# Optimization experiments

Measured on AMD Instinct MI355X. Metric: run time of the kernel, lower is better.

## Reference

```python
import jax, jax.numpy as jnp
import numpy as np

TAU_FILTER_INV = 1000.0
DT = 0.001
# decay = 1 - alpha = exp(-dt * tau_filter_inv)
DECAY = float(np.exp(-DT * TAU_FILTER_INV))


def setup_inputs() -> dict:
    key = jax.random.key(0)
    k1, k2, k3 = jax.random.split(key, 3)
    T, B, I, O = 2048, 32, 256, 256
    input_tensor = jax.random.normal(k1, (T, B, I), dtype=jnp.float32)
    # Linear weight init mimics uniform(-k, k), k = sqrt(1/input_size)
    k = float(np.sqrt(1.0 / I))
    W = jax.random.uniform(k2, (O, I), dtype=jnp.float32, minval=-k, maxval=k)
    b = jax.random.uniform(k3, (O,), dtype=jnp.float32, minval=-k, maxval=k)
    return {"input_tensor": input_tensor, "W": W, "b": b}


def reference(input_tensor, W, b):
    # Dense projection: [T, B, I] @ [I, O] -> [T, B, O]
    y = jnp.einsum("tbi,oi->tbo", input_tensor, W) + b
    decay = jnp.asarray(DECAY, dtype=y.dtype)

    # s(t) = y(t) + decay * s(t-1); s(0) = y(0) (init state 0)
    def step(s, x):
        s = x + decay * s
        return s, s

    _, out = jax.lax.scan(step, jnp.zeros_like(y[0]), y)
    return out
```

## Files before the change

### kernel.cpp

```cpp
#include <hip/hip_runtime.h>
#include <cstddef>


#define DECAY  0.36787944117144233f
#define D10    4.5399929762484854e-5f
#define INV1MD 1.5819767068693265f

typedef __attribute__((ext_vector_type(8))) short short8;
typedef __attribute__((ext_vector_type(4))) short short4v;
typedef __attribute__((ext_vector_type(4))) float f32x4;

static constexpr int T_DIM = 2048, B_DIM = 32, K_DIM = 256, N_DIM = 256;
static constexpr int M_DIM = T_DIM * B_DIM;
static constexpr int PS  = 32768;
static constexpr int TCH = 32;

__device__ __forceinline__ float bfbits2f(unsigned short u) {
  unsigned int x = ((unsigned int)u) << 16;
  return __builtin_bit_cast(float, x);
}
__device__ __forceinline__ short f2bf_s(float f) {
  __bf16 h = (__bf16)f;
  return __builtin_bit_cast(short, h);
}

__global__ void k_split_w(const float* __restrict__ W, short* __restrict__ Wh) {
  const int o = blockIdx.x, i = threadIdx.x;
  size_t off = (size_t)(o >> 7) * PS + (i >> 5) * 4096 + ((i >> 3) & 3) * 1024 +
               (o & 127) * 8 + (i & 7);
  Wh[off] = f2bf_s(W[o * 256 + i]);
}

__global__ __launch_bounds__(256, 5)
void k_fused(const float* __restrict__ X, const short* __restrict__ Wth,
             const float* __restrict__ bias, float* __restrict__ out) {
  __shared__ __align__(16) char ldsA[16384];
  __shared__ __align__(16) short cbh[4 * 256];
  __shared__ float cfac[TCH];

  const int tid  = threadIdx.x;
  const int lane = tid & 63;
  const int wv   = tid >> 6;
  const int c    = blockIdx.x;
  const int b    = blockIdx.y;
  const int t0   = c * TCH;
  const int ch4  = lane * 4;

  const int row16 = lane & 15;
  const int kq    = lane >> 4;
  const int cg    = wv;
  const short* Wp = Wth + (size_t)(cg >> 1) * PS;
  const int wbase = kq * 1024 + ((cg & 1) * 64 + row16) * 8;

  if (tid < TCH)
    cfac[tid] = (1.f - __expf(-(float)(t0 + tid + 1))) * INV1MD;

  f32x4 y[10];
  {
    const int ts = t0 + wv * 10 - 8;
    if (ts >= 0) {
      const float* xp = X + (size_t)ts * 8192 + b * 256 + ch4;
      #pragma unroll
      for (int j = 0; j < 10; ++j)
        y[j] = *reinterpret_cast<const f32x4*>(xp + (size_t)j * 8192);
      f32x4 s = {0.f, 0.f, 0.f, 0.f};
      #pragma unroll
      for (int j = 0; j < 10; ++j) {
        #pragma unroll
        for (int e = 0; e < 4; ++e) s[e] = fmaf(DECAY, s[e], y[j][e]);
        y[j] = s;
      }
    } else {
      f32x4 x0 = *reinterpret_cast<const f32x4*>(X + b * 256 + ch4);
      f32x4 x1 = *reinterpret_cast<const f32x4*>(X + 8192 + b * 256 + ch4);
      y[8] = x0;
      #pragma unroll
      for (int e = 0; e < 4; ++e) y[9][e] = fmaf(DECAY, x0[e], x1[e]);
    }
  }
  {
    short4v cv;
    #pragma unroll
    for (int e = 0; e < 4; ++e) cv[e] = f2bf_s(y[9][e]);
    *reinterpret_cast<short4v*>(&cbh[wv * 256 + ch4]) = cv;
  }

  short8 bh[2][4];
  #pragma unroll
  for (int ct = 0; ct < 4; ++ct)
    bh[0][ct] = *reinterpret_cast<const short8*>(Wp + wbase + ct * 128);
  __builtin_amdgcn_sched_barrier(0);

  __syncthreads();

  f32x4 cin = {0.f, 0.f, 0.f, 0.f};
  {
    float m = 1.f;
    for (int v = wv - 1; v >= 0; --v) {
      short4v cv = *reinterpret_cast<const short4v*>(&cbh[v * 256 + ch4]);
      #pragma unroll
      for (int e = 0; e < 4; ++e)
        cin[e] = fmaf(bfbits2f((unsigned short)cv[e]), m, cin[e]);
      m *= D10;
    }
  }

  {
    static constexpr float DP[10] = {
        0.36787944117144233f,  0.1353352832366127f,   0.049787068367863944f,
        0.018315638888734179f, 0.006737946999085467f, 0.0024787521766663585f,
        0.0009118819655545162f, 0.00033546262790251185f,
        1.2340980408667956e-4f, 4.5399929762484854e-5f};
    #pragma unroll
    for (int j = 0; j < 10; ++j) {
      const int r = wv * 10 + j - 8;
      if (r >= 0) {
        short4v hv;
        #pragma unroll
        for (int e = 0; e < 4; ++e)
          hv[e] = f2bf_s(fmaf(cin[e], DP[j], y[j][e]));
        const int byte = (r * 512 + ch4 * 2) ^ ((r & 7) << 4);
        *reinterpret_cast<short4v*>(ldsA + byte) = hv;
      }
    }
  }
  __syncthreads();

  f32x4 acc[2][4] = {};
  #pragma unroll
  for (int kt = 0; kt < 8; ++kt) {
    const int cur = kt & 1;
    if (kt < 7) {
      #pragma unroll
      for (int ct = 0; ct < 4; ++ct)
        bh[cur ^ 1][ct] = *reinterpret_cast<const short8*>(
            Wp + (kt + 1) * 4096 + wbase + ct * 128);
      __builtin_amdgcn_sched_barrier(0);
    }
    short8 ah0, ah1;
    {
      const int b0 = (row16 * 512 + kt * 64 + kq * 16) ^ ((row16 & 7) << 4);
      const int row1 = row16 + 16;
      const int b1 = (row1 * 512 + kt * 64 + kq * 16) ^ ((row1 & 7) << 4);
      ah0 = *reinterpret_cast<const short8*>(ldsA + b0);
      ah1 = *reinterpret_cast<const short8*>(ldsA + b1);
    }
    #pragma unroll
    for (int ct = 0; ct < 4; ++ct) {
      acc[0][ct] = __builtin_amdgcn_mfma_f32_16x16x32_bf16(
          ah0, bh[cur][ct], acc[0][ct], 0, 0, 0);
      acc[1][ct] = __builtin_amdgcn_mfma_f32_16x16x32_bf16(
          ah1, bh[cur][ct], acc[1][ct], 0, 0, 0);
    }
  }

  const f32x4* bias4 = reinterpret_cast<const f32x4*>(bias);
  #pragma unroll
  for (int p = 0; p < 2; ++p) {
    __syncthreads();
    #pragma unroll
    for (int ct = 0; ct < 4; ++ct)
      #pragma unroll
      for (int j = 0; j < 4; ++j) {
        const int rowh = kq * 4 + j;
        const int col  = cg * 64 + ct * 16 + row16;
        const int byte = (rowh * 1024 + col * 4) ^ ((rowh & 7) << 4);
        *reinterpret_cast<float*>(ldsA + byte) = acc[p][ct][j];
      }
    __syncthreads();
    #pragma unroll
    for (int q = 0; q < 4; ++q) {
      const int idx  = tid + q * 256;
      const int rowh = idx >> 6;
      const int colc = idx & 63;
      const int byte = (idx * 16) ^ ((rowh & 7) << 4);
      f32x4 yv = *reinterpret_cast<const f32x4*>(ldsA + byte);
      const int row = p * 16 + rowh;
      f32x4 bv = bias4[colc];
      const float cf = cfac[row];
      f32x4 r;
      #pragma unroll
      for (int e = 0; e < 4; ++e) r[e] = fmaf(bv[e], cf, yv[e]);
      __builtin_nontemporal_store(
          r, reinterpret_cast<f32x4*>(out + ((size_t)(t0 + row) * 32 + b) * 256 +
                                      colc * 4));
    }
  }
}

__global__ void k_fb_gemm(const float* __restrict__ X, const float* __restrict__ W,
                          const float* __restrict__ bias, float* __restrict__ Y) {
  size_t idx = (size_t)blockIdx.x * 256 + threadIdx.x;
  int o = (int)(idx & 255);
  size_t m = idx >> 8;
  const float* x = X + m * 256;
  const float* w = W + (size_t)o * 256;
  float s = bias[o];
  for (int k = 0; k < 256; ++k) s = fmaf(x[k], w[k], s);
  Y[idx] = s;
}
__global__ void k_fb_scan(float* __restrict__ Y) {
  int ch = blockIdx.x * 256 + threadIdx.x;
  float s = 0.f;
  float* p = Y + ch;
  for (int t = 0; t < 2048; ++t) { s = fmaf(DECAY, s, *p); *p = s; p += 8192; }
}

extern "C" void kernel_launch(void* const* d_in, const int* in_sizes, int n_in,
                              void* d_out, int out_size, void* d_ws, size_t ws_size,
                              hipStream_t stream) {
  const float* X    = (const float*)d_in[0];
  const float* W    = (const float*)d_in[1];
  const float* bias = (const float*)d_in[2];
  float* out = (float*)d_out;

  const size_t w_elems = (size_t)N_DIM * K_DIM;
  const size_t need    = w_elems * sizeof(short);

  if (ws_size >= need) {
    short* Wh = (short*)d_ws;
    k_split_w<<<N_DIM, 256, 0, stream>>>(W, Wh);
    k_fused<<<dim3(T_DIM / TCH, B_DIM), 256, 0, stream>>>(X, Wh, bias, out);
  } else {
    k_fb_gemm<<<M_DIM, 256, 0, stream>>>(X, W, bias, out);
    k_fb_scan<<<32, 256, 0, stream>>>(out);
  }
}
```

Before: 39.24 us.

## Warp-specialize fused scan-GEMM into producer/consumer pipeline over multiple chunks

Each block now processes four 32-step time chunks with 512 threads. Four producer waves load and scan the input chunk while four consumer waves run the MFMA GEMM and epilogue for the previous chunk, using double-buffered LDS and a ring of chunk carries. The warm-up overlap shrinks: carry-in now comes from the previous three 8-step segments, plus a warm-up only at the block boundary, instead of a 10-step overlap per wave. This is meant to overlap memory loads with MFMA work and cut redundant input reads, at the cost of more LDS, fewer blocks (512 total) and an extra barrier per stage.

```diff
diff --git a/kernel.cpp b/kernel.cpp
--- a/kernel.cpp
+++ b/kernel.cpp
@@ -3,7 +3,8 @@
 
 
 #define DECAY  0.36787944117144233f
-#define D10    4.5399929762484854e-5f
+#define D8     3.3546262790251185e-4f
+#define D16    1.1253517471925912e-7f
 #define INV1MD 1.5819767068693265f
 
 typedef __attribute__((ext_vector_type(8))) short short8;
@@ -13,7 +14,8 @@
 static constexpr int T_DIM = 2048, B_DIM = 32, K_DIM = 256, N_DIM = 256;
 static constexpr int M_DIM = T_DIM * B_DIM;
 static constexpr int PS  = 32768;
-static constexpr int TCH = 32;
+static constexpr int CR  = 32;
+static constexpr int NCH = 4;
 
 __device__ __forceinline__ float bfbits2f(unsigned short u) {
   unsigned int x = ((unsigned int)u) << 16;
@@ -31,160 +33,179 @@
   Wh[off] = f2bf_s(W[o * 256 + i]);
 }
 
-__global__ __launch_bounds__(256, 5)
+__global__ __launch_bounds__(512, 4)
 void k_fused(const float* __restrict__ X, const short* __restrict__ Wth,
              const float* __restrict__ bias, float* __restrict__ out) {
-  __shared__ __align__(16) char ldsA[16384];
-  __shared__ __align__(16) short cbh[4 * 256];
-  __shared__ float cfac[TCH];
+  __shared__ __align__(16) char ldsA[32768];
+  __shared__ __align__(16) char ldsY[32768];
+  __shared__ __align__(16) short cring[8 * 256];
 
   const int tid  = threadIdx.x;
   const int lane = tid & 63;
   const int wv   = tid >> 6;
-  const int c    = blockIdx.x;
+  const int c2   = blockIdx.x;
   const int b    = blockIdx.y;
-  const int t0   = c * TCH;
-  const int ch4  = lane * 4;
-
+  const int t0B  = c2 * (CR * NCH);
+
+  const int ch4   = lane * 4;
   const int row16 = lane & 15;
   const int kq    = lane >> 4;
-  const int cg    = wv;
-  const short* Wp = Wth + (size_t)(cg >> 1) * PS;
-  const int wbase = kq * 1024 + ((cg & 1) * 64 + row16) * 8;
-
-  if (tid < TCH)
-    cfac[tid] = (1.f - __expf(-(float)(t0 + tid + 1))) * INV1MD;
-
-  f32x4 y[10];
-  {
-    const int ts = t0 + wv * 10 - 8;
-    if (ts >= 0) {
-      const float* xp = X + (size_t)ts * 8192 + b * 256 + ch4;
-      #pragma unroll
-      for (int j = 0; j < 10; ++j)
-        y[j] = *reinterpret_cast<const f32x4*>(xp + (size_t)j * 8192);
-      f32x4 s = {0.f, 0.f, 0.f, 0.f};
-      #pragma unroll
-      for (int j = 0; j < 10; ++j) {
-        #pragma unroll
-        for (int e = 0; e < 4; ++e) s[e] = fmaf(DECAY, s[e], y[j][e]);
-        y[j] = s;
-      }
-    } else {
-      f32x4 x0 = *reinterpret_cast<const f32x4*>(X + b * 256 + ch4);
-      f32x4 x1 = *reinterpret_cast<const f32x4*>(X + 8192 + b * 256 + ch4);
-      y[8] = x0;
-      #pragma unroll
-      for (int e = 0; e < 4; ++e) y[9][e] = fmaf(DECAY, x0[e], x1[e]);
+  const bool isP  = (wv < 4);
+  const int p     = wv;
+
+  static constexpr float DP[8] = {
+      0.36787944117144233f,  0.1353352832366127f,  0.049787068367863944f,
+      0.018315638888734179f, 0.006737946999085467f, 0.0024787521766663585f,
+      0.0009118819655545162f, 3.3546262790251185e-4f};
+
+  for (int s = 0; s <= NCH; ++s) {
+    f32x4 y[8];
+    f32x4 cwarm = {0.f, 0.f, 0.f, 0.f};
+    f32x4 acc[2][4] = {};
+
+    if (isP) {
+      if (s < NCH) {
+        const int r0 = t0B + s * CR + p * 8;
+        const float* xp = X + (size_t)r0 * 8192 + b * 256 + ch4;
+        if (s == 0 && p == 0 && c2 > 0) {
+          const float* wp = xp - (size_t)8 * 8192;
+          #pragma unroll
+          for (int j = 0; j < 8; ++j) {
+            f32x4 xw = *reinterpret_cast<const f32x4*>(wp + (size_t)j * 8192);
+            #pragma unroll
+            for (int e = 0; e < 4; ++e) cwarm[e] = fmaf(DECAY, cwarm[e], xw[e]);
+          }
+        }
+        #pragma unroll
+        for (int j = 0; j < 8; ++j)
+          y[j] = *reinterpret_cast<const f32x4*>(xp + (size_t)j * 8192);
+        f32x4 sa = {0.f, 0.f, 0.f, 0.f};
+        #pragma unroll
+        for (int j = 0; j < 8; ++j) {
+          #pragma unroll
+          for (int e = 0; e < 4; ++e) sa[e] = fmaf(DECAY, sa[e], y[j][e]);
+          y[j] = sa;
+        }
+        short4v cv;
+        #pragma unroll
+        for (int e = 0; e < 4; ++e) cv[e] = f2bf_s(y[7][e]);
+        *reinterpret_cast<short4v*>(&cring[((4 * s + p) & 7) * 256 + ch4]) = cv;
+      }
+    } else if (s >= 1) {
+      const int c   = s - 1;
+      const int cw  = wv - 4;
+      const char* A = ldsA + (c & 1) * 16384;
+      const short* Wp = Wth + (size_t)(cw >> 1) * PS;
+      const int wbase = kq * 1024 + ((cw & 1) * 64 + row16) * 8;
+
+      short8 bh[2][4];
+      #pragma unroll
+      for (int ct = 0; ct < 4; ++ct)
+        bh[0][ct] = *reinterpret_cast<const short8*>(Wp + wbase + ct * 128);
+      __builtin_amdgcn_sched_barrier(0);
+
+      #pragma unroll
+      for (int kt = 0; kt < 8; ++kt) {
+        const int cur = kt & 1;
+        if (kt < 7) {
+          #pragma unroll
+          for (int ct = 0; ct < 4; ++ct)
+            bh[cur ^ 1][ct] = *reinterpret_cast<const short8*>(
+                Wp + (kt + 1) * 4096 + wbase + ct * 128);
+          __builtin_amdgcn_sched_barrier(0);
+        }
+        short8 ah0, ah1;
+        {
+          const int b0 = (row16 * 512 + kt * 64 + kq * 16) ^ ((row16 & 7) << 4);
+          const int r1 = row16 + 16;
+          const int b1 = (r1 * 512 + kt * 64 + kq * 16) ^ ((r1 & 7) << 4);
+          ah0 = *reinterpret_cast<const short8*>(A + b0);
+          ah1 = *reinterpret_cast<const short8*>(A + b1);
+        }
+        #pragma unroll
+        for (int ct = 0; ct < 4; ++ct) {
+          acc[0][ct] = __builtin_amdgcn_mfma_f32_16x16x32_bf16(
+              ah0, bh[cur][ct], acc[0][ct], 0, 0, 0);
+          acc[1][ct] = __builtin_amdgcn_mfma_f32_16x16x32_bf16(
+              ah1, bh[cur][ct], acc[1][ct], 0, 0, 0);
+        }
+      }
+      #pragma unroll
+      for (int rf = 0; rf < 2; ++rf)
+        #pragma unroll
+        for (int ct = 0; ct < 4; ++ct)
+          #pragma unroll
+          for (int j = 0; j < 4; ++j) {
+            const int rowh = rf * 16 + kq * 4 + j;
+            const int col  = cw * 64 + ct * 16 + row16;
+            const int byte = (rowh * 1024 + col * 4) ^ ((rowh & 7) << 4);
+            *reinterpret_cast<float*>(ldsY + byte) = acc[rf][ct][j];
+          }
     }
-  }
-  {
-    short4v cv;
-    #pragma unroll
-    for (int e = 0; e < 4; ++e) cv[e] = f2bf_s(y[9][e]);
-    *reinterpret_cast<short4v*>(&cbh[wv * 256 + ch4]) = cv;
-  }
-
-  short8 bh[2][4];
-  #pragma unroll
-  for (int ct = 0; ct < 4; ++ct)
-    bh[0][ct] = *reinterpret_cast<const short8*>(Wp + wbase + ct * 128);
-  __builtin_amdgcn_sched_barrier(0);
-
-  __syncthreads();
-
-  f32x4 cin = {0.f, 0.f, 0.f, 0.f};
-  {
-    float m = 1.f;
-    for (int v = wv - 1; v >= 0; --v) {
-      short4v cv = *reinterpret_cast<const short4v*>(&cbh[v * 256 + ch4]);
-      #pragma unroll
-      for (int e = 0; e < 4; ++e)
-        cin[e] = fmaf(bfbits2f((unsigned short)cv[e]), m, cin[e]);
-      m *= D10;
+    __syncthreads();
+
+    if (isP) {
+      if (s < NCH) {
+        f32x4 cin = cwarm;
+        {
+          const int g1 = 4 * s + p - 1;
+          if (g1 >= 0) {
+            short4v cv = *reinterpret_cast<const short4v*>(
+                &cring[(g1 & 7) * 256 + ch4]);
+            #pragma unroll
+            for (int e = 0; e < 4; ++e)
+              cin[e] += bfbits2f((unsigned short)cv[e]);
+          }
+          if (g1 >= 1) {
+            short4v cv = *reinterpret_cast<const short4v*>(
+                &cring[((g1 - 1) & 7) * 256 + ch4]);
+            #pragma unroll
+            for (int e = 0; e < 4; ++e)
+              cin[e] = fmaf(bfbits2f((unsigned short)cv[e]), D8, cin[e]);
+          }
+          if (g1 >= 2) {
+            short4v cv = *reinterpret_cast<const short4v*>(
+                &cring[((g1 - 2) & 7) * 256 + ch4]);
+            #pragma unroll
+            for (int e = 0; e < 4; ++e)
+              cin[e] = fmaf(bfbits2f((unsigned short)cv[e]), D16, cin[e]);
+          }
+        }
+        char* A = ldsA + (s & 1) * 16384;
+        #pragma unroll
+        for (int j = 0; j < 8; ++j) {
+          const int row = p * 8 + j;
+          short4v hv;
+          #pragma unroll
+          for (int e = 0; e < 4; ++e)
+            hv[e] = f2bf_s(fmaf(cin[e], DP[j], y[j][e]));
+          const int byte = (row * 512 + ch4 * 2) ^ ((row & 7) << 4);
+          *reinterpret_cast<short4v*>(A + byte) = hv;
+        }
+      }
+    } else if (s >= 1) {
+      const int t0c  = t0B + (s - 1) * CR;
+      const int ctid = tid - 256;
+      const f32x4* bias4 = reinterpret_cast<const f32x4*>(bias);
+      #pragma unroll
+      for (int q = 0; q < 8; ++q) {
+        const int idx  = ctid + q * 256;
+        const int rowh = idx >> 6;
+        const int colc = idx & 63;
+        const int byte = (idx * 16) ^ ((rowh & 7) << 4);
+        f32x4 yv = *reinterpret_cast<const f32x4*>(ldsY + byte);
+        f32x4 bv = bias4[colc];
+        const float cf =
+            (1.f - __expf(-(float)(t0c + rowh + 1))) * INV1MD;
+        f32x4 r;
+        #pragma unroll
+        for (int e = 0; e < 4; ++e) r[e] = fmaf(bv[e], cf, yv[e]);
+        __builtin_nontemporal_store(
+            r, reinterpret_cast<f32x4*>(
+                   out + ((size_t)(t0c + rowh) * 32 + b) * 256 + colc * 4));
+      }
     }
-  }
-
-  {
-    static constexpr float DP[10] = {
-        0.36787944117144233f,  0.1353352832366127f,   0.049787068367863944f,
-        0.018315638888734179f, 0.006737946999085467f, 0.0024787521766663585f,
-        0.0009118819655545162f, 0.00033546262790251185f,
-        1.2340980408667956e-4f, 4.5399929762484854e-5f};
-    #pragma unroll
-    for (int j = 0; j < 10; ++j) {
-      const int r = wv * 10 + j - 8;
-      if (r >= 0) {
-        short4v hv;
-        #pragma unroll
-        for (int e = 0; e < 4; ++e)
-          hv[e] = f2bf_s(fmaf(cin[e], DP[j], y[j][e]));
-        const int byte = (r * 512 + ch4 * 2) ^ ((r & 7) << 4);
-        *reinterpret_cast<short4v*>(ldsA + byte) = hv;
-      }
-    }
-  }
-  __syncthreads();
-
-  f32x4 acc[2][4] = {};
-  #pragma unroll
-  for (int kt = 0; kt < 8; ++kt) {
-    const int cur = kt & 1;
-    if (kt < 7) {
-      #pragma unroll
-      for (int ct = 0; ct < 4; ++ct)
-        bh[cur ^ 1][ct] = *reinterpret_cast<const short8*>(
-            Wp + (kt + 1) * 4096 + wbase + ct * 128);
-      __builtin_amdgcn_sched_barrier(0);
-    }
-    short8 ah0, ah1;
-    {
-      const int b0 = (row16 * 512 + kt * 64 + kq * 16) ^ ((row16 & 7) << 4);
-      const int row1 = row16 + 16;
-      const int b1 = (row1 * 512 + kt * 64 + kq * 16) ^ ((row1 & 7) << 4);
-      ah0 = *reinterpret_cast<const short8*>(ldsA + b0);
-      ah1 = *reinterpret_cast<const short8*>(ldsA + b1);
-    }
-    #pragma unroll
-    for (int ct = 0; ct < 4; ++ct) {
-      acc[0][ct] = __builtin_amdgcn_mfma_f32_16x16x32_bf16(
-          ah0, bh[cur][ct], acc[0][ct], 0, 0, 0);
-      acc[1][ct] = __builtin_amdgcn_mfma_f32_16x16x32_bf16(
-          ah1, bh[cur][ct], acc[1][ct], 0, 0, 0);
-    }
-  }
-
-  const f32x4* bias4 = reinterpret_cast<const f32x4*>(bias);
-  #pragma unroll
-  for (int p = 0; p < 2; ++p) {
     __syncthreads();
-    #pragma unroll
-    for (int ct = 0; ct < 4; ++ct)
-      #pragma unroll
-      for (int j = 0; j < 4; ++j) {
-        const int rowh = kq * 4 + j;
-        const int col  = cg * 64 + ct * 16 + row16;
-        const int byte = (rowh * 1024 + col * 4) ^ ((rowh & 7) << 4);
-        *reinterpret_cast<float*>(ldsA + byte) = acc[p][ct][j];
-      }
-    __syncthreads();
-    #pragma unroll
-    for (int q = 0; q < 4; ++q) {
-      const int idx  = tid + q * 256;
-      const int rowh = idx >> 6;
-      const int colc = idx & 63;
-      const int byte = (idx * 16) ^ ((rowh & 7) << 4);
-      f32x4 yv = *reinterpret_cast<const f32x4*>(ldsA + byte);
-      const int row = p * 16 + rowh;
-      f32x4 bv = bias4[colc];
-      const float cf = cfac[row];
-      f32x4 r;
-      #pragma unroll
-      for (int e = 0; e < 4; ++e) r[e] = fmaf(bv[e], cf, yv[e]);
-      __builtin_nontemporal_store(
-          r, reinterpret_cast<f32x4*>(out + ((size_t)(t0 + row) * 32 + b) * 256 +
-                                      colc * 4));
-    }
   }
 }
 
@@ -220,7 +241,8 @@
   if (ws_size >= need) {
     short* Wh = (short*)d_ws;
     k_split_w<<<N_DIM, 256, 0, stream>>>(W, Wh);
-    k_fused<<<dim3(T_DIM / TCH, B_DIM), 256, 0, stream>>>(X, Wh, bias, out);
+    k_fused<<<dim3(T_DIM / (CR * NCH), B_DIM), 512, 0, stream>>>(X, Wh, bias,
+                                                                 out);
   } else {
     k_fb_gemm<<<M_DIM, 256, 0, stream>>>(X, W, bias, out);
     k_fb_scan<<<32, 256, 0, stream>>>(out);
```

After: 96.60 us. 2.46x slower.
